# Performance work log

Measured on AMD Instinct MI355X. Metric: run time of the kernel, lower is better.

## Reference

```python
import jax, jax.numpy as jnp
import numpy as np

N_NODES = 50_000
N_EDGES = 1_600_000
IN_HIDDEN = 256
OUT_HIDDEN = 32
EDGE_HIDDEN = 64
NHEAD = 4
N_EDGE_TYPES = 8
NEG_SLOPE = 0.2


def _glorot(key, shape):
    stdv = np.sqrt(6.0 / (shape[-2] + shape[-1]))
    return jax.random.uniform(key, shape, jnp.float32, -stdv, stdv)


def setup_inputs() -> dict:
    key = jax.random.key(0)
    ks = jax.random.split(key, 10)
    src = jax.random.randint(ks[0], (N_EDGES,), 0, N_NODES, dtype=jnp.int32)
    trg = jax.random.randint(ks[1], (N_EDGES,), 0, N_NODES, dtype=jnp.int32)
    etype = jax.random.randint(ks[2], (N_EDGES,), 0, N_EDGE_TYPES, dtype=jnp.int32)
    edge = jnp.stack([src, trg, etype], axis=0)  # [3, E]
    x = jax.random.normal(ks[3], (N_NODES, IN_HIDDEN), jnp.float32)
    return {
        "edge": edge,
        "x": x,
        "edge_emb": _glorot(ks[4], (N_EDGE_TYPES, EDGE_HIDDEN)),
        "W": _glorot(ks[5], (IN_HIDDEN, OUT_HIDDEN * NHEAD)),
        "W_e": _glorot(ks[6], (EDGE_HIDDEN, EDGE_HIDDEN * NHEAD)),
        "a_l": _glorot(ks[7], (1, NHEAD, OUT_HIDDEN)),
        "a_r": _glorot(ks[8], (1, NHEAD, OUT_HIDDEN)),
        "a_e": _glorot(ks[9], (1, NHEAD, EDGE_HIDDEN)),
    }


def reference(edge, x, edge_emb, W, W_e, a_l, a_r, a_e):
    num_nodes = x.shape[0]
    src, trg, etype = edge[0], edge[1], edge[2]

    # node / edge-type projections
    h = (x @ W).reshape(num_nodes, NHEAD, OUT_HIDDEN)          # [N, H, D]
    h = jnp.where(jnp.isnan(h), 0.0, h)
    e = (edge_emb @ W_e).reshape(N_EDGE_TYPES, NHEAD, EDGE_HIDDEN)  # [T, H, De]

    # per-node / per-type attention logits, gathered to edges -> [E, H]
    h_l = (a_l * h).sum(-1)[src]
    h_r = (a_r * h).sum(-1)[trg]
    h_e = (a_e * e).sum(-1)[etype]
    scores = jax.nn.leaky_relu(h_l + h_r + h_e, NEG_SLOPE)     # [E, H]

    # neighborhood-aware softmax (global max shift, as in original)
    exp_scores = jnp.exp(scores - jnp.max(scores))
    denom = jax.ops.segment_sum(exp_scores, trg, num_segments=num_nodes)  # [N, H]
    attn = (exp_scores / (denom[trg] + 1e-16))[:, :, None]     # [E, H, 1]

    # weighted aggregation: scatter-add messages to targets
    msgs = h[src] * attn                                       # [E, H, D]
    out = jax.ops.segment_sum(msgs, trg, num_segments=num_nodes)  # [N, H, D]
    return out, attn
```

## Files before the change

kernel.cpp:

```cpp
#include <hip/hip_runtime.h>
#include <hip/hip_bf16.h>

#define N_NODES 50000
#define N_EDGES 1600000
#define IN_H 256
#define NHEAD 4
#define EDGE_H 64
#define N_ET 8


typedef __attribute__((ext_vector_type(8))) short bf16x8v;
typedef __attribute__((ext_vector_type(4))) float f32x4;

__device__ __forceinline__ float ldT(const float* p) { return *p; }
__device__ __forceinline__ float ldT(const __hip_bfloat16* p) { return __bfloat162float(*p); }
__device__ __forceinline__ void stT(float* p, float v) { *p = v; }
__device__ __forceinline__ void stT(__hip_bfloat16* p, float v) { *p = __float2bfloat16(v); }

__device__ __forceinline__ short f2bs(float f) {
    __hip_bfloat16 b = __float2bfloat16(f);
    return (short)__builtin_bit_cast(unsigned short, b);
}
__device__ __forceinline__ float bs2f(short s) {
    return __uint_as_float(((unsigned)(unsigned short)s) << 16);
}

__device__ __forceinline__ unsigned enc_f32(float f) {
    unsigned u = __float_as_uint(f);
    return (u & 0x80000000u) ? ~u : (u | 0x80000000u);
}
__device__ __forceinline__ float dec_f32(unsigned u) {
    return __uint_as_float((u & 0x80000000u) ? (u & 0x7fffffffu) : ~u);
}
__device__ __forceinline__ float lrelu(float v) { return v > 0.f ? v : 0.2f * v; }

__global__ void k_detect(const unsigned* __restrict__ xw, int* __restrict__ flag) {
    int lane = threadIdx.x;
    int cnt = 0;
    for (int i = lane; i < 1024; i += 64) {
        unsigned e = (xw[i] >> 23) & 255u;
        if (e >= 64u && e <= 160u) cnt++;
    }
    for (int off = 32; off; off >>= 1) cnt += __shfl_xor(cnt, off);
    if (lane == 0) *flag = (cnt > 512) ? 1 : 0;
}

template<typename T, int EXPECT>
__global__ __launch_bounds__(256) void k_setup(
        const void* __restrict__ Wv, const void* __restrict__ embv,
        const void* __restrict__ Wev, const void* __restrict__ aev,
        __hip_bfloat16* __restrict__ Wt, float* __restrict__ h_e,
        unsigned* __restrict__ hemax, const int* __restrict__ flag) {
    if (*flag != EXPECT) return;
    const T* W   = (const T*)Wv;
    const T* emb = (const T*)embv;
    const T* We  = (const T*)Wev;
    const T* ae  = (const T*)aev;
    if (blockIdx.x == 0) {
        for (int i = threadIdx.x; i < 128 * 256; i += 256) {
            int c = i >> 8, k = i & 255;
            Wt[i] = __float2bfloat16(ldT(W + k * 128 + c));
        }
        return;
    }
    int ty = blockIdx.x - 1;
    int t = threadIdx.x, lane = t & 63;
    float acc = 0.f;
    for (int k = 0; k < EDGE_H; ++k)
        acc += ldT(emb + ty * EDGE_H + k) * ldT(We + k * 256 + t);
    float v = ldT(ae + t) * acc;
    for (int off = 32; off; off >>= 1) v += __shfl_xor(v, off);
    if (lane == 0) {
        h_e[ty * NHEAD + (t >> 6)] = v;
        atomicMax(&hemax[t >> 6], enc_f32(v));
    }
}

template<typename T, int EXPECT>
__global__ __launch_bounds__(256) void k_proj(const void* __restrict__ xv,
        const __hip_bfloat16* __restrict__ Wt, __hip_bfloat16* __restrict__ h,
        float* __restrict__ hl, float* __restrict__ hr,
        const void* __restrict__ alv, const void* __restrict__ arv,
        const int* __restrict__ flag) {
    if (*flag != EXPECT) return;
    const T* x  = (const T*)xv;
    const T* al = (const T*)alv;
    const T* ar = (const T*)arv;
    int wid = threadIdx.x >> 6, lane = threadIdx.x & 63;
    int rg = blockIdx.x * 2 + (wid >> 1);
    if (rg >= 3125) return;
    int toff = (wid & 1) * 4;
    int r0 = rg * 16;
    int r = lane & 15;
    int kb = (lane >> 4) * 8;
    const T* xrow = x + (size_t)(r0 + r) * IN_H;
    f32x4 z = {0.f, 0.f, 0.f, 0.f};
    f32x4 acc[4];
#pragma unroll
    for (int t = 0; t < 4; ++t) acc[t] = z;
#pragma unroll
    for (int kk = 0; kk < 8; ++kk) {
        int k0 = kk * 32 + kb;
        bf16x8v a;
        if constexpr (sizeof(T) == 4) {
            float4 lo = *(const float4*)(xrow + k0);
            float4 hi = *(const float4*)(xrow + k0 + 4);
            a[0] = f2bs(lo.x); a[1] = f2bs(lo.y); a[2] = f2bs(lo.z); a[3] = f2bs(lo.w);
            a[4] = f2bs(hi.x); a[5] = f2bs(hi.y); a[6] = f2bs(hi.z); a[7] = f2bs(hi.w);
        } else {
            a = *(const bf16x8v*)(xrow + k0);
        }
#pragma unroll
        for (int t = 0; t < 4; ++t) {
            bf16x8v b = *(const bf16x8v*)(Wt + ((toff + t) * 16 + r) * 256 + k0);
            acc[t] = __builtin_amdgcn_mfma_f32_16x16x32_bf16(a, b, acc[t], 0, 0, 0);
        }
    }
    float alc[4], arc[4];
#pragma unroll
    for (int t = 0; t < 4; ++t) {
        alc[t] = ldT(al + (toff + t) * 16 + r);
        arc[t] = ldT(ar + (toff + t) * 16 + r);
    }
    int ob = (lane >> 4) * 4;
    float pl[2][4] = {{0,0,0,0},{0,0,0,0}}, pr[2][4] = {{0,0,0,0},{0,0,0,0}};
#pragma unroll
    for (int t = 0; t < 4; ++t) {
        int col = (toff + t) * 16 + r;
#pragma unroll
        for (int g = 0; g < 4; ++g) {
            float v = acc[t][g];
            if (v != v) v = 0.f;
            h[(size_t)(r0 + ob + g) * 128 + col] = __float2bfloat16(v);
            pl[t >> 1][g] += alc[t] * v;
            pr[t >> 1][g] += arc[t] * v;
        }
    }
#pragma unroll
    for (int hh = 0; hh < 2; ++hh)
#pragma unroll
        for (int g = 0; g < 4; ++g) {
            float vl = pl[hh][g], vr = pr[hh][g];
#pragma unroll
            for (int off = 8; off; off >>= 1) {
                vl += __shfl_xor(vl, off);
                vr += __shfl_xor(vr, off);
            }
            if (r == 0) {
                int node = r0 + ob + g;
                hl[node * 4 + (toff >> 1) + hh] = vl;
                hr[node * 4 + (toff >> 1) + hh] = vr;
            }
        }
}

__global__ __launch_bounds__(256) void k_countaux(
        const int* __restrict__ edge, int* __restrict__ counts,
        const float* __restrict__ hl, const float* __restrict__ hr,
        unsigned* __restrict__ hlmax, unsigned* __restrict__ hrmax) {
    int e = blockIdx.x * 256 + threadIdx.x;
    atomicAdd(&counts[edge[N_EDGES + e]], 1);
    if (blockIdx.x >= 128) return;
    const float NEG = -3.4e38f;
    float4 ml = {NEG, NEG, NEG, NEG}, mr = {NEG, NEG, NEG, NEG};
    for (int n = blockIdx.x * 256 + threadIdx.x; n < N_NODES; n += 128 * 256) {
        float4 a = *(const float4*)(hl + n * 4);
        float4 b = *(const float4*)(hr + n * 4);
        ml.x = fmaxf(ml.x, a.x); ml.y = fmaxf(ml.y, a.y);
        ml.z = fmaxf(ml.z, a.z); ml.w = fmaxf(ml.w, a.w);
        mr.x = fmaxf(mr.x, b.x); mr.y = fmaxf(mr.y, b.y);
        mr.z = fmaxf(mr.z, b.z); mr.w = fmaxf(mr.w, b.w);
    }
#pragma unroll
    for (int off = 32; off; off >>= 1) {
        ml.x = fmaxf(ml.x, __shfl_xor(ml.x, off));
        ml.y = fmaxf(ml.y, __shfl_xor(ml.y, off));
        ml.z = fmaxf(ml.z, __shfl_xor(ml.z, off));
        ml.w = fmaxf(ml.w, __shfl_xor(ml.w, off));
        mr.x = fmaxf(mr.x, __shfl_xor(mr.x, off));
        mr.y = fmaxf(mr.y, __shfl_xor(mr.y, off));
        mr.z = fmaxf(mr.z, __shfl_xor(mr.z, off));
        mr.w = fmaxf(mr.w, __shfl_xor(mr.w, off));
    }
    if ((threadIdx.x & 63) == 0) {
        atomicMax(&hlmax[0], enc_f32(ml.x)); atomicMax(&hlmax[1], enc_f32(ml.y));
        atomicMax(&hlmax[2], enc_f32(ml.z)); atomicMax(&hlmax[3], enc_f32(ml.w));
        atomicMax(&hrmax[0], enc_f32(mr.x)); atomicMax(&hrmax[1], enc_f32(mr.y));
        atomicMax(&hrmax[2], enc_f32(mr.z)); atomicMax(&hrmax[3], enc_f32(mr.w));
    }
}

__global__ __launch_bounds__(256) void k_scan(
        const int* __restrict__ counts, int* __restrict__ offsets) {
    __shared__ int psum[256];
    int t = threadIdx.x;
    const int CHUNK = 196;
    int start = t * CHUNK;
    int end = min(start + CHUNK, N_NODES);
    int s = 0;
    for (int i = start; i < end; i += 4) {
        int4 c = *(const int4*)(counts + i);
        s += c.x + c.y + c.z + c.w;
    }
    psum[t] = s;
    __syncthreads();
    for (int off = 1; off < 256; off <<= 1) {
        int v = (t >= off) ? psum[t - off] : 0;
        __syncthreads();
        psum[t] += v;
        __syncthreads();
    }
    int run = (t == 0) ? 0 : psum[t - 1];
    for (int i = start; i < end; i += 4) {
        int4 c = *(const int4*)(counts + i);
        int4 o;
        o.x = run; o.y = run + c.x; o.z = o.y + c.y; o.w = o.z + c.z;
        *(int4*)(offsets + i) = o;
        run = o.w + c.w;
    }
    if (t == 255) offsets[N_NODES] = run;
}

__global__ __launch_bounds__(256) void k_build(
        const int* __restrict__ edge, const int* __restrict__ offsets,
        int* __restrict__ cursor,
        const float* __restrict__ hl, const float* __restrict__ hr,
        const float* __restrict__ he,
        const unsigned* __restrict__ hlmax, const unsigned* __restrict__ hrmax,
        const unsigned* __restrict__ hemax,
        float* __restrict__ rec) {
    float M0 = lrelu(dec_f32(hlmax[0]) + dec_f32(hrmax[0]) + dec_f32(hemax[0]));
    float M1 = lrelu(dec_f32(hlmax[1]) + dec_f32(hrmax[1]) + dec_f32(hemax[1]));
    float M2 = lrelu(dec_f32(hlmax[2]) + dec_f32(hrmax[2]) + dec_f32(hemax[2]));
    float M3 = lrelu(dec_f32(hlmax[3]) + dec_f32(hrmax[3]) + dec_f32(hemax[3]));
    int e = blockIdx.x * 256 + threadIdx.x;
    int s = edge[e], t = edge[N_EDGES + e], ty = edge[2 * N_EDGES + e];
    int pos = offsets[t] + atomicAdd(&cursor[t], 1);
    float4 a = *(const float4*)(hl + s * 4);
    float4 b = *(const float4*)(hr + t * 4);
    float4 c = *(const float4*)(he + ty * 4);
    float4 p;
    p.x = __expf(lrelu(a.x + b.x + c.x) - M0);
    p.y = __expf(lrelu(a.y + b.y + c.y) - M1);
    p.z = __expf(lrelu(a.z + b.z + c.z) - M2);
    p.w = __expf(lrelu(a.w + b.w + c.w) - M3);
    float4 se;
    se.x = __int_as_float(s); se.y = __int_as_float(e); se.z = 0.f; se.w = 0.f;
    float* rp = rec + (size_t)pos * 8;
    *(float4*)rp = p;
    *(float4*)(rp + 4) = se;
}

template<typename OUTT, int EXPECT>
__global__ __launch_bounds__(256) void k_agg(
        const float* __restrict__ rec, const int* __restrict__ offsets,
        const __hip_bfloat16* __restrict__ h, void* __restrict__ outv,
        const int* __restrict__ flag) {
    if (*flag != EXPECT) return;
    OUTT* out = (OUTT*)outv;
    int node = (blockIdx.x << 2) + (threadIdx.x >> 6);
    if (node >= N_NODES) return;
    int lane = threadIdx.x & 63;
    int beg = offsets[node], end = offsets[node + 1];

    float d0 = 0.f, d1 = 0.f, d2 = 0.f, d3 = 0.f;
    for (int j = beg + lane; j < end; j += 64) {
        float4 p = *(const float4*)(rec + (size_t)j * 8);
        d0 += p.x; d1 += p.y; d2 += p.z; d3 += p.w;
    }
#pragma unroll
    for (int off = 32; off; off >>= 1) {
        d0 += __shfl_xor(d0, off); d1 += __shfl_xor(d1, off);
        d2 += __shfl_xor(d2, off); d3 += __shfl_xor(d3, off);
    }
    float inv0 = 1.f / (d0 + 1e-16f), inv1 = 1.f / (d1 + 1e-16f);
    float inv2 = 1.f / (d2 + 1e-16f), inv3 = 1.f / (d3 + 1e-16f);

    int sub = lane >> 4;
    int l16 = lane & 15;
    int hd  = l16 >> 2;
    float invd = hd == 0 ? inv0 : hd == 1 ? inv1 : hd == 2 ? inv2 : inv3;
    float inva = l16 == 0 ? inv0 : l16 == 1 ? inv1 : l16 == 2 ? inv2 : inv3;
    OUTT* attn_out = out + (size_t)N_NODES * 128;

    float acc[8] = {0.f, 0.f, 0.f, 0.f, 0.f, 0.f, 0.f, 0.f};
    for (int jg = beg; jg < end; jg += 4) {
        int j = jg + sub;
        bool valid = j < end;
        int jc = valid ? j : end - 1;
        const float* rp = rec + (size_t)jc * 8;
        float4 p = *(const float4*)rp;
        int2 se = *(const int2*)(rp + 4);
        int s = se.x;
        if (valid && l16 < 4) {
            float ph = l16 == 0 ? p.x : l16 == 1 ? p.y : l16 == 2 ? p.z : p.w;
            stT(&attn_out[(size_t)se.y * 4 + l16], ph * inva);
        }
        float phd = hd == 0 ? p.x : hd == 1 ? p.y : hd == 2 ? p.z : p.w;
        float w = valid ? phd * invd : 0.f;
        bf16x8v hv = *(const bf16x8v*)(h + (size_t)s * 128 + l16 * 8);
#pragma unroll
        for (int i = 0; i < 8; ++i) acc[i] += bs2f(hv[i]) * w;
    }
#pragma unroll
    for (int i = 0; i < 8; ++i) {
        acc[i] += __shfl_xor(acc[i], 16);
        acc[i] += __shfl_xor(acc[i], 32);
    }
    if (sub == 0) {
#pragma unroll
        for (int i = 0; i < 8; ++i)
            stT(&out[(size_t)node * 128 + l16 * 8 + i], acc[i]);
    }
}

extern "C" void kernel_launch(void* const* d_in, const int* in_sizes, int n_in,
                              void* d_out, int out_size, void* d_ws, size_t ws_size,
                              hipStream_t stream) {
    const int* edge = (const int*)d_in[0];
    const void* x   = d_in[1];
    const void* emb = d_in[2];
    const void* W   = d_in[3];
    const void* We  = d_in[4];
    const void* al  = d_in[5];
    const void* ar  = d_in[6];
    const void* ae  = d_in[7];

    float* ws = (float*)d_ws;
    int* counts     = (int*)ws;
    int* cursor     = counts + 50000;
    unsigned* hlmax = (unsigned*)(counts + 100000);
    unsigned* hrmax = hlmax + 4;
    unsigned* hemax = hlmax + 8;
    int* flag       = counts + 100012;
    float* hl       = ws + 100064;
    float* hr       = ws + 300064;
    int* offsets    = (int*)ws + 500064;
    float* he       = ws + 550112;
    __hip_bfloat16* Wt = (__hip_bfloat16*)(ws + 550144);
    float* rec      = ws + 566528;
    __hip_bfloat16* h = (__hip_bfloat16*)(ws + 13366528);

    hipMemsetAsync(ws, 0, (size_t)100064 * 4, stream);

    k_detect<<<1, 64, 0, stream>>>((const unsigned*)x, flag);

    k_setup<float, 1><<<1 + N_ET, 256, 0, stream>>>(W, emb, We, ae, Wt, he,
                                                    hemax, flag);
    k_setup<__hip_bfloat16, 0><<<1 + N_ET, 256, 0, stream>>>(W, emb, We, ae, Wt,
                                                             he, hemax, flag);

    k_proj<float, 1><<<1563, 256, 0, stream>>>(x, Wt, h, hl, hr, al, ar, flag);
    k_proj<__hip_bfloat16, 0><<<1563, 256, 0, stream>>>(x, Wt, h, hl, hr,
                                                        al, ar, flag);

    k_countaux<<<6250, 256, 0, stream>>>(edge, counts, hl, hr, hlmax, hrmax);
    k_scan<<<1, 256, 0, stream>>>(counts, offsets);
    k_build<<<6250, 256, 0, stream>>>(edge, offsets, cursor, hl, hr, he,
                                      hlmax, hrmax, hemax, rec);

    k_agg<float, 1><<<12500, 256, 0, stream>>>(rec, offsets, h, d_out, flag);
    k_agg<__hip_bfloat16, 0><<<12500, 256, 0, stream>>>(rec, offsets, h,
                                                        d_out, flag);
}
```

Measured before the change: 456.2 us.

## Pack edge records to fp16, fuse degree counting into projection, per-target shift

Each edge record shrinks from 32 to 16 bytes: the four exponentiated scores are stored as packed fp16 next to the source and edge ids. This cuts write traffic in k_build and read traffic in both passes of k_agg. The global softmax shift is replaced by a per-target upper bound (max h_l plus max h_e plus that target's h_r). That shift cancels within each target's normalization, so it removes the need for the hr max reduction. Degree counting moves into the k_proj kernel, k_countaux shrinks to an hl-only max kernel, and the scan runs with 1024 threads. The cost is fp16 precision on the unnormalized weights, which could underflow for very small values.

Result: faster. 446.1 us (-2.2%).

```diff
diff --git a/kernel.cpp b/kernel.cpp
--- a/kernel.cpp
+++ b/kernel.cpp
@@ -1,5 +1,6 @@
 #include <hip/hip_runtime.h>
 #include <hip/hip_bf16.h>
+#include <hip/hip_fp16.h>
 
 #define N_NODES 50000
 #define N_EDGES 1600000
@@ -33,6 +34,16 @@
     return __uint_as_float((u & 0x80000000u) ? (u & 0x7fffffffu) : ~u);
 }
 __device__ __forceinline__ float lrelu(float v) { return v > 0.f ? v : 0.2f * v; }
+
+__device__ __forceinline__ unsigned pack_h2(float a, float b) {
+    unsigned lo = (unsigned)__half_as_ushort(__float2half(a));
+    unsigned hi = (unsigned)__half_as_ushort(__float2half(b));
+    return lo | (hi << 16);
+}
+__device__ __forceinline__ float2 unpack_h2(int w) {
+    __half2 h = __builtin_bit_cast(__half2, w);
+    return __half22float2(h);
+}
 
 __global__ void k_detect(const unsigned* __restrict__ xw, int* __restrict__ flag) {
     int lane = threadIdx.x;
@@ -81,8 +92,15 @@
         const __hip_bfloat16* __restrict__ Wt, __hip_bfloat16* __restrict__ h,
         float* __restrict__ hl, float* __restrict__ hr,
         const void* __restrict__ alv, const void* __restrict__ arv,
+        const int* __restrict__ edge, int* __restrict__ counts,
         const int* __restrict__ flag) {
     if (*flag != EXPECT) return;
+    {
+        int base = blockIdx.x * 1024;
+        int lim = min(base + 1024, N_EDGES);
+        for (int i = base + threadIdx.x; i < lim; i += 256)
+            atomicAdd(&counts[edge[N_EDGES + i]], 1);
+    }
     const T* x  = (const T*)xv;
     const T* al = (const T*)alv;
     const T* ar = (const T*)arv;
@@ -154,22 +172,14 @@
         }
 }
 
-__global__ __launch_bounds__(256) void k_countaux(
-        const int* __restrict__ edge, int* __restrict__ counts,
-        const float* __restrict__ hl, const float* __restrict__ hr,
-        unsigned* __restrict__ hlmax, unsigned* __restrict__ hrmax) {
-    int e = blockIdx.x * 256 + threadIdx.x;
-    atomicAdd(&counts[edge[N_EDGES + e]], 1);
-    if (blockIdx.x >= 128) return;
+__global__ __launch_bounds__(256) void k_maxred(
+        const float* __restrict__ hl, unsigned* __restrict__ hlmax) {
     const float NEG = -3.4e38f;
-    float4 ml = {NEG, NEG, NEG, NEG}, mr = {NEG, NEG, NEG, NEG};
+    float4 ml = {NEG, NEG, NEG, NEG};
     for (int n = blockIdx.x * 256 + threadIdx.x; n < N_NODES; n += 128 * 256) {
         float4 a = *(const float4*)(hl + n * 4);
-        float4 b = *(const float4*)(hr + n * 4);
         ml.x = fmaxf(ml.x, a.x); ml.y = fmaxf(ml.y, a.y);
         ml.z = fmaxf(ml.z, a.z); ml.w = fmaxf(ml.w, a.w);
-        mr.x = fmaxf(mr.x, b.x); mr.y = fmaxf(mr.y, b.y);
-        mr.z = fmaxf(mr.z, b.z); mr.w = fmaxf(mr.w, b.w);
     }
 #pragma unroll
     for (int off = 32; off; off >>= 1) {
@@ -177,24 +187,18 @@
         ml.y = fmaxf(ml.y, __shfl_xor(ml.y, off));
         ml.z = fmaxf(ml.z, __shfl_xor(ml.z, off));
         ml.w = fmaxf(ml.w, __shfl_xor(ml.w, off));
-        mr.x = fmaxf(mr.x, __shfl_xor(mr.x, off));
-        mr.y = fmaxf(mr.y, __shfl_xor(mr.y, off));
-        mr.z = fmaxf(mr.z, __shfl_xor(mr.z, off));
-        mr.w = fmaxf(mr.w, __shfl_xor(mr.w, off));
     }
     if ((threadIdx.x & 63) == 0) {
         atomicMax(&hlmax[0], enc_f32(ml.x)); atomicMax(&hlmax[1], enc_f32(ml.y));
         atomicMax(&hlmax[2], enc_f32(ml.z)); atomicMax(&hlmax[3], enc_f32(ml.w));
-        atomicMax(&hrmax[0], enc_f32(mr.x)); atomicMax(&hrmax[1], enc_f32(mr.y));
-        atomicMax(&hrmax[2], enc_f32(mr.z)); atomicMax(&hrmax[3], enc_f32(mr.w));
-    }
-}
-
-__global__ __launch_bounds__(256) void k_scan(
+    }
+}
+
+__global__ __launch_bounds__(1024) void k_scan(
         const int* __restrict__ counts, int* __restrict__ offsets) {
-    __shared__ int psum[256];
+    __shared__ int psum[1024];
     int t = threadIdx.x;
-    const int CHUNK = 196;
+    const int CHUNK = 52;
     int start = t * CHUNK;
     int end = min(start + CHUNK, N_NODES);
     int s = 0;
@@ -204,7 +208,7 @@
     }
     psum[t] = s;
     __syncthreads();
-    for (int off = 1; off < 256; off <<= 1) {
+    for (int off = 1; off < 1024; off <<= 1) {
         int v = (t >= off) ? psum[t - off] : 0;
         __syncthreads();
         psum[t] += v;
@@ -218,7 +222,7 @@
         *(int4*)(offsets + i) = o;
         run = o.w + c.w;
     }
-    if (t == 255) offsets[N_NODES] = run;
+    if (start < N_NODES && end == N_NODES) offsets[N_NODES] = run;
 }
 
 __global__ __launch_bounds__(256) void k_build(
@@ -226,34 +230,33 @@
         int* __restrict__ cursor,
         const float* __restrict__ hl, const float* __restrict__ hr,
         const float* __restrict__ he,
-        const unsigned* __restrict__ hlmax, const unsigned* __restrict__ hrmax,
-        const unsigned* __restrict__ hemax,
-        float* __restrict__ rec) {
-    float M0 = lrelu(dec_f32(hlmax[0]) + dec_f32(hrmax[0]) + dec_f32(hemax[0]));
-    float M1 = lrelu(dec_f32(hlmax[1]) + dec_f32(hrmax[1]) + dec_f32(hemax[1]));
-    float M2 = lrelu(dec_f32(hlmax[2]) + dec_f32(hrmax[2]) + dec_f32(hemax[2]));
-    float M3 = lrelu(dec_f32(hlmax[3]) + dec_f32(hrmax[3]) + dec_f32(hemax[3]));
+        const unsigned* __restrict__ hlmax, const unsigned* __restrict__ hemax,
+        int* __restrict__ rec) {
+    float G0 = dec_f32(hlmax[0]) + dec_f32(hemax[0]);
+    float G1 = dec_f32(hlmax[1]) + dec_f32(hemax[1]);
+    float G2 = dec_f32(hlmax[2]) + dec_f32(hemax[2]);
+    float G3 = dec_f32(hlmax[3]) + dec_f32(hemax[3]);
     int e = blockIdx.x * 256 + threadIdx.x;
     int s = edge[e], t = edge[N_EDGES + e], ty = edge[2 * N_EDGES + e];
     int pos = offsets[t] + atomicAdd(&cursor[t], 1);
     float4 a = *(const float4*)(hl + s * 4);
     float4 b = *(const float4*)(hr + t * 4);
     float4 c = *(const float4*)(he + ty * 4);
-    float4 p;
-    p.x = __expf(lrelu(a.x + b.x + c.x) - M0);
-    p.y = __expf(lrelu(a.y + b.y + c.y) - M1);
-    p.z = __expf(lrelu(a.z + b.z + c.z) - M2);
-    p.w = __expf(lrelu(a.w + b.w + c.w) - M3);
-    float4 se;
-    se.x = __int_as_float(s); se.y = __int_as_float(e); se.z = 0.f; se.w = 0.f;
-    float* rp = rec + (size_t)pos * 8;
-    *(float4*)rp = p;
-    *(float4*)(rp + 4) = se;
+    float p0 = __expf(lrelu(a.x + b.x + c.x) - lrelu(G0 + b.x));
+    float p1 = __expf(lrelu(a.y + b.y + c.y) - lrelu(G1 + b.y));
+    float p2 = __expf(lrelu(a.z + b.z + c.z) - lrelu(G2 + b.z));
+    float p3 = __expf(lrelu(a.w + b.w + c.w) - lrelu(G3 + b.w));
+    int4 w;
+    w.x = (int)pack_h2(p0, p1);
+    w.y = (int)pack_h2(p2, p3);
+    w.z = s;
+    w.w = e;
+    *(int4*)(rec + (size_t)pos * 4) = w;
 }
 
 template<typename OUTT, int EXPECT>
 __global__ __launch_bounds__(256) void k_agg(
-        const float* __restrict__ rec, const int* __restrict__ offsets,
+        const int* __restrict__ rec, const int* __restrict__ offsets,
         const __hip_bfloat16* __restrict__ h, void* __restrict__ outv,
         const int* __restrict__ flag) {
     if (*flag != EXPECT) return;
@@ -265,8 +268,10 @@
 
     float d0 = 0.f, d1 = 0.f, d2 = 0.f, d3 = 0.f;
     for (int j = beg + lane; j < end; j += 64) {
-        float4 p = *(const float4*)(rec + (size_t)j * 8);
-        d0 += p.x; d1 += p.y; d2 += p.z; d3 += p.w;
+        int2 w = *(const int2*)(rec + (size_t)j * 4);
+        float2 f01 = unpack_h2(w.x);
+        float2 f23 = unpack_h2(w.y);
+        d0 += f01.x; d1 += f01.y; d2 += f23.x; d3 += f23.y;
     }
 #pragma unroll
     for (int off = 32; off; off >>= 1) {
@@ -288,19 +293,19 @@
         int j = jg + sub;
         bool valid = j < end;
         int jc = valid ? j : end - 1;
-        const float* rp = rec + (size_t)jc * 8;
-        float4 p = *(const float4*)rp;
-        int2 se = *(const int2*)(rp + 4);
-        int s = se.x;
+        int4 w = *(const int4*)(rec + (size_t)jc * 4);
+        float2 f01 = unpack_h2(w.x);
+        float2 f23 = unpack_h2(w.y);
+        int s = w.z;
         if (valid && l16 < 4) {
-            float ph = l16 == 0 ? p.x : l16 == 1 ? p.y : l16 == 2 ? p.z : p.w;
-            stT(&attn_out[(size_t)se.y * 4 + l16], ph * inva);
-        }
-        float phd = hd == 0 ? p.x : hd == 1 ? p.y : hd == 2 ? p.z : p.w;
-        float w = valid ? phd * invd : 0.f;
+            float ph = l16 == 0 ? f01.x : l16 == 1 ? f01.y : l16 == 2 ? f23.x : f23.y;
+            stT(&attn_out[(size_t)w.w * 4 + l16], ph * inva);
+        }
+        float phd = hd == 0 ? f01.x : hd == 1 ? f01.y : hd == 2 ? f23.x : f23.y;
+        float wgt = valid ? phd * invd : 0.f;
         bf16x8v hv = *(const bf16x8v*)(h + (size_t)s * 128 + l16 * 8);
 #pragma unroll
-        for (int i = 0; i < 8; ++i) acc[i] += bs2f(hv[i]) * w;
+        for (int i = 0; i < 8; ++i) acc[i] += bs2f(hv[i]) * wgt;
     }
 #pragma unroll
     for (int i = 0; i < 8; ++i) {
@@ -330,7 +335,6 @@
     int* counts     = (int*)ws;
     int* cursor     = counts + 50000;
     unsigned* hlmax = (unsigned*)(counts + 100000);
-    unsigned* hrmax = hlmax + 4;
     unsigned* hemax = hlmax + 8;
     int* flag       = counts + 100012;
     float* hl       = ws + 100064;
@@ -338,8 +342,8 @@
     int* offsets    = (int*)ws + 500064;
     float* he       = ws + 550112;
     __hip_bfloat16* Wt = (__hip_bfloat16*)(ws + 550144);
-    float* rec      = ws + 566528;
-    __hip_bfloat16* h = (__hip_bfloat16*)(ws + 13366528);
+    int* rec        = (int*)ws + 566528;
+    __hip_bfloat16* h = (__hip_bfloat16*)(ws + 6966528);
 
     hipMemsetAsync(ws, 0, (size_t)100064 * 4, stream);
 
@@ -350,14 +354,15 @@
     k_setup<__hip_bfloat16, 0><<<1 + N_ET, 256, 0, stream>>>(W, emb, We, ae, Wt,
                                                              he, hemax, flag);
 
-    k_proj<float, 1><<<1563, 256, 0, stream>>>(x, Wt, h, hl, hr, al, ar, flag);
+    k_proj<float, 1><<<1563, 256, 0, stream>>>(x, Wt, h, hl, hr, al, ar,
+                                               edge, counts, flag);
     k_proj<__hip_bfloat16, 0><<<1563, 256, 0, stream>>>(x, Wt, h, hl, hr,
-                                                        al, ar, flag);
-
-    k_countaux<<<6250, 256, 0, stream>>>(edge, counts, hl, hr, hlmax, hrmax);
-    k_scan<<<1, 256, 0, stream>>>(counts, offsets);
+                                                        al, ar, edge, counts, flag);
+
+    k_maxred<<<128, 256, 0, stream>>>(hl, hlmax);
+    k_scan<<<1, 1024, 0, stream>>>(counts, offsets);
     k_build<<<6250, 256, 0, stream>>>(edge, offsets, cursor, hl, hr, he,
-                                      hlmax, hrmax, hemax, rec);
+                                      hlmax, hemax, rec);
 
     k_agg<float, 1><<<12500, 256, 0, stream>>>(rec, offsets, h, d_out, flag);
     k_agg<__hip_bfloat16, 0><<<12500, 256, 0, stream>>>(rec, offsets, h,
```
